# Kernel optimization log

Measured on AMD Instinct MI355X. Metric: run time of the kernel, lower is better.

The kernel has to match this reference:

```python
import jax, jax.numpy as jnp
import numpy as np

B, T, D, H = 8, 1024, 1024, 16

def setup_inputs() -> dict:
    key = jax.random.key(0)
    k1, k2, k3, k4, k5 = jax.random.split(key, 5)
    x = jax.random.normal(k1, (B, T, D), dtype=jnp.float32)
    mask = jnp.tril(jnp.ones((T, T), dtype=bool))[None, None]  # [1,1,T,T] causal
    s = 0.02
    W_attn = jax.random.normal(k2, (D, 3 * D), dtype=jnp.float32) * s
    b_attn = jnp.zeros((3 * D,), dtype=jnp.float32)
    W_proj = jax.random.normal(k3, (D, D), dtype=jnp.float32) * s
    b_proj = jnp.zeros((D,), dtype=jnp.float32)
    return {"x": x, "mask": mask, "W_attn": W_attn, "b_attn": b_attn,
            "W_proj": W_proj, "b_proj": b_proj}

def reference(x, mask, W_attn, b_attn, W_proj, b_proj):
    num_heads = H
    b, t, d = x.shape
    hd = d // num_heads
    qkv = x @ W_attn + b_attn                      # [b,t,3d]
    q, k, v = jnp.split(qkv, 3, axis=-1)
    def to_heads(a):
        return a.reshape(b, t, num_heads, hd).transpose(0, 2, 1, 3)  # [b,h,t,hd]
    q, k, v = to_heads(q), to_heads(k), to_heads(v)
    scale = 1.0 / jnp.sqrt(jnp.float32(hd))
    attn = jnp.einsum('bhqd,bhkd->bhqk', q, k) * scale
    attn = jnp.where(mask, attn, jnp.finfo(jnp.float32).min)
    attn = jax.nn.softmax(attn, axis=-1)
    o = jnp.einsum('bhqk,bhkd->bhqd', attn, v)
    o = o.transpose(0, 2, 1, 3).reshape(b, t, d)   # [b,t,d]
    return o @ W_proj + b_proj
```

## Files before the change

### kernel.cpp

```cpp
#include <hip/hip_runtime.h>
#include <cstdint>


typedef __attribute__((ext_vector_type(8))) short bf16x8;
typedef __attribute__((ext_vector_type(4))) float f32x4;

__device__ __forceinline__ short f2b(float x) {
  unsigned u = __builtin_bit_cast(unsigned, x);
  u += 0x7fffu + ((u >> 16) & 1u);
  return (short)(u >> 16);
}

__device__ __forceinline__ void gl2lds16(short* l, const short* g) {
  __builtin_amdgcn_global_load_lds(
      (const __attribute__((address_space(1))) void*)g,
      (__attribute__((address_space(3))) void*)l, 16, 0, 0);
}


__global__ void f32_to_bf16_vec(const float* __restrict__ in,
                                short* __restrict__ outb, int n4) {
  int i = blockIdx.x * 256 + threadIdx.x;
  if (i >= n4) return;
  float4 v = ((const float4*)in)[i];
  short4 o;
  o.x = f2b(v.x); o.y = f2b(v.y); o.z = f2b(v.z); o.w = f2b(v.w);
  ((short4*)outb)[i] = o;
}

__global__ void transpose_f32_bf16(const float* __restrict__ in,
                                   short* __restrict__ out, int R, int C) {
  __shared__ float tile[32][33];
  int c0 = blockIdx.x * 32, r0 = blockIdx.y * 32;
  int tx = threadIdx.x, ty = threadIdx.y;
#pragma unroll
  for (int i = 0; i < 32; i += 8)
    tile[ty + i][tx] = in[(long)(r0 + ty + i) * C + c0 + tx];
  __syncthreads();
#pragma unroll
  for (int i = 0; i < 32; i += 8)
    out[(long)(c0 + ty + i) * R + r0 + tx] = f2b(tile[tx][ty + i]);
}


template <int EPI>
__global__ __launch_bounds__(256, 3) void gemm_bt(
    const short* __restrict__ A, const short* __restrict__ Bt,
    const float* __restrict__ bias, float* __restrict__ outF,
    short* __restrict__ qh, short* __restrict__ kh, short* __restrict__ vT,
    int M, int N, int K) {
  __shared__ short At[128 * 64];
  __shared__ short Bl[128 * 64];
  const int t = threadIdx.x;
  const int wave = t >> 6, lane = t & 63;
  const int quad = lane >> 4, l15 = lane & 15;
  const int wr = wave >> 1, wc = wave & 1;
  const int m0 = blockIdx.y * 128, n0 = blockIdx.x * 128;

  f32x4 acc[4][4] = {};

  const int srow = t >> 3;
  const int sch0 = t & 7;

  for (int k0 = 0; k0 < K; k0 += 64) {
    __syncthreads();
#pragma unroll
    for (int c = 0; c < 4; ++c) {
      int row = c * 32 + srow;
      int ch = sch0 ^ (row & 7);
      gl2lds16(At + (c * 256 + t) * 8, A + (long)(m0 + row) * K + k0 + ch * 8);
      gl2lds16(Bl + (c * 256 + t) * 8, Bt + (long)(n0 + row) * K + k0 + ch * 8);
    }
    asm volatile("s_waitcnt vmcnt(0)" ::: "memory");
    __syncthreads();

#pragma unroll
    for (int s = 0; s < 2; ++s) {
      const int cx = (s * 4 + quad) ^ (l15 & 7);
      bf16x8 af[4], bfr[4];
#pragma unroll
      for (int i = 0; i < 4; ++i)
        af[i] = *(const bf16x8*)(At + (wr * 64 + i * 16 + l15) * 64 + cx * 8);
#pragma unroll
      for (int j = 0; j < 4; ++j)
        bfr[j] = *(const bf16x8*)(Bl + (wc * 64 + j * 16 + l15) * 64 + cx * 8);
#pragma unroll
      for (int i = 0; i < 4; ++i)
#pragma unroll
        for (int j = 0; j < 4; ++j)
          acc[i][j] = __builtin_amdgcn_mfma_f32_16x16x32_bf16(af[i], bfr[j],
                                                              acc[i][j], 0, 0, 0);
    }
  }

  if (EPI == 1) {
#pragma unroll
    for (int j = 0; j < 4; ++j) {
      int col = n0 + wc * 64 + j * 16 + l15;
      float bv = bias[col];
#pragma unroll
      for (int i = 0; i < 4; ++i)
#pragma unroll
        for (int r = 0; r < 4; ++r) {
          int row = m0 + wr * 64 + i * 16 + quad * 4 + r;
          outF[(long)row * N + col] = acc[i][j][r] + bv;
        }
    }
  } else {
    const int sec = n0 >> 10;
    const int b = m0 >> 10;
#pragma unroll
    for (int j = 0; j < 4; ++j) {
      int col = n0 + wc * 64 + j * 16 + l15;
      float bv = bias[col];
      int d = col & 1023, h = d >> 6, dh = d & 63;
      if (sec == 2) {
        long base = ((long)(b * 16 + h) * 64 + dh) * 1024;
#pragma unroll
        for (int i = 0; i < 4; ++i) {
          int tt0 = (m0 & 1023) + wr * 64 + i * 16 + quad * 4;
          short4 v;
          v.x = f2b(acc[i][j][0] + bv);
          v.y = f2b(acc[i][j][1] + bv);
          v.z = f2b(acc[i][j][2] + bv);
          v.w = f2b(acc[i][j][3] + bv);
          *(short4*)(vT + base + tt0) = v;
        }
      } else {
        short* dst = (sec == 0) ? qh : kh;
        long hbase = ((long)(b * 16 + h) * 1024) * 64 + dh;
#pragma unroll
        for (int i = 0; i < 4; ++i)
#pragma unroll
          for (int r = 0; r < 4; ++r) {
            int tt = (m0 & 1023) + wr * 64 + i * 16 + quad * 4 + r;
            dst[hbase + (long)tt * 64] = f2b(acc[i][j][r] + bv);
          }
      }
    }
  }
}


__global__ __launch_bounds__(256, 2) void attn_kernel(
    const short* __restrict__ qh, const short* __restrict__ kh,
    const short* __restrict__ vT, short* __restrict__ attout) {
  __shared__ short Kb[2][64 * 64];
  __shared__ short Vb[2][64 * 64];
  __shared__ short P_lds[4][16][64];
  const int p = blockIdx.x;
  const int bh = blockIdx.y;
  const int t = threadIdx.x;
  const int wave = t >> 6, lane = t & 63, quad = lane >> 4, l15 = lane & 15;
  const short* q_head = qh + (long)bh * 1024 * 64;
  const short* k_head = kh + (long)bh * 1024 * 64;
  const short* v_head = vT + (long)bh * 64 * 1024;
  const int b_ = bh >> 4, h_ = bh & 15;
  const float sl = 0.125f * 1.44269504089f;

  const int qt[4] = {p, 7 - p, 8 + p, 15 - p};

  auto stage = [&](int kt, int buf) {
    const int kk0 = kt * 64;
#pragma unroll
    for (int i = 0; i < 2; ++i) {
      int s = i * 256 + t;
      int row = s >> 3, cg = (s & 7) ^ (row & 7);
      gl2lds16(&Kb[buf][s * 8], k_head + (kk0 + row) * 64 + cg * 8);
    }
#pragma unroll
    for (int i = 0; i < 2; ++i) {
      int s = i * 256 + t;
      int row = s >> 3, cg = (s & 7) ^ (row & 7);
      gl2lds16(&Vb[buf][s * 8], v_head + row * 1024 + kk0 + cg * 8);
    }
  };

  bf16x8 qf[4][2];
#pragma unroll
  for (int i = 0; i < 4; ++i) {
    int qb = qt[i] * 64 + wave * 16;
#pragma unroll
    for (int s = 0; s < 2; ++s)
      qf[i][s] = *(const bf16x8*)(q_head + (qb + l15) * 64 + s * 32 + quad * 8);
  }

  float l[4][4] = {};
  f32x4 o[4][4] = {};

  stage(0, 0);
  __syncthreads();

  const int nkt = qt[3] + 1;

#pragma unroll 1
  for (int kt = 0; kt < nkt; ++kt) {
    const int buf = kt & 1;
    const short* Kt = Kb[buf];
    const short* Vt = Vb[buf];

    bf16x8 kfr[4][2], vfr[4][2];
#pragma unroll
    for (int jj = 0; jj < 4; ++jj) {
      int row = jj * 16 + l15;
#pragma unroll
      for (int s = 0; s < 2; ++s) {
        int off = ((s * 4 + quad) ^ (row & 7)) * 8;
        kfr[jj][s] = *(const bf16x8*)(Kt + row * 64 + off);
        vfr[jj][s] = *(const bf16x8*)(Vt + row * 64 + off);
      }
    }

    if (kt + 1 < nkt) stage(kt + 1, buf ^ 1);

#pragma unroll
    for (int i = 0; i < 4; ++i) {
      if (kt <= qt[i]) {
        f32x4 s4[4] = {};
#pragma unroll
        for (int jj = 0; jj < 4; ++jj) {
          s4[jj] = __builtin_amdgcn_mfma_f32_16x16x32_bf16(qf[i][0], kfr[jj][0],
                                                           s4[jj], 0, 0, 0);
          s4[jj] = __builtin_amdgcn_mfma_f32_16x16x32_bf16(qf[i][1], kfr[jj][1],
                                                           s4[jj], 0, 0, 0);
        }
        const bool diag = (kt == qt[i]);
        const int qb = qt[i] * 64 + wave * 16;
#pragma unroll
        for (int jj = 0; jj < 4; ++jj) {
          int key = kt * 64 + jj * 16 + l15;
          int ch = jj * 2 + (l15 >> 3), co = l15 & 7;
#pragma unroll
          for (int r = 0; r < 4; ++r) {
            int row = quad * 4 + r;
            float sv = s4[jj][r] * sl;
            if (diag && key > qb + row) sv = -1e30f;
            float e = __builtin_amdgcn_exp2f(sv);
            l[i][r] += e;
            P_lds[wave][row][(ch ^ (row & 7)) * 8 + co] = f2b(e);
          }
        }
        asm volatile("s_waitcnt lgkmcnt(0)" ::: "memory");
        bf16x8 pf[2];
#pragma unroll
        for (int s = 0; s < 2; ++s)
          pf[s] =
              *(const bf16x8*)(&P_lds[wave][l15][((s * 4 + quad) ^ (l15 & 7)) * 8]);
#pragma unroll
        for (int dj = 0; dj < 4; ++dj) {
          o[i][dj] = __builtin_amdgcn_mfma_f32_16x16x32_bf16(pf[0], vfr[dj][0],
                                                             o[i][dj], 0, 0, 0);
          o[i][dj] = __builtin_amdgcn_mfma_f32_16x16x32_bf16(pf[1], vfr[dj][1],
                                                             o[i][dj], 0, 0, 0);
        }
      }
    }
    __syncthreads();
  }

#pragma unroll
  for (int off = 1; off < 16; off <<= 1)
#pragma unroll
    for (int i = 0; i < 4; ++i)
#pragma unroll
      for (int r = 0; r < 4; ++r) l[i][r] += __shfl_xor(l[i][r], off);

  const int erow = lane >> 3, ech = lane & 7;
#pragma unroll
  for (int i = 0; i < 4; ++i) {
    float inv[4];
#pragma unroll
    for (int r = 0; r < 4; ++r) inv[r] = __builtin_amdgcn_rcpf(l[i][r]);
    const int qb = qt[i] * 64 + wave * 16;
#pragma unroll
    for (int dj = 0; dj < 4; ++dj) {
      int ch = dj * 2 + (l15 >> 3), co = l15 & 7;
#pragma unroll
      for (int r = 0; r < 4; ++r) {
        int row = quad * 4 + r;
        P_lds[wave][row][(ch ^ (row & 7)) * 8 + co] = f2b(o[i][dj][r] * inv[r]);
      }
    }
    asm volatile("s_waitcnt lgkmcnt(0)" ::: "memory");
#pragma unroll
    for (int pass = 0; pass < 2; ++pass) {
      int row = pass * 8 + erow;
      bf16x8 v = *(const bf16x8*)(&P_lds[wave][row][(ech ^ (row & 7)) * 8]);
      long g = (long)b_ * 1024 + qb + row;
      *(bf16x8*)(attout + g * 1024 + h_ * 64 + ech * 8) = v;
    }
    asm volatile("s_waitcnt lgkmcnt(0)" ::: "memory");
  }
}


extern "C" void kernel_launch(void* const* d_in, const int* in_sizes, int n_in,
                              void* d_out, int out_size, void* d_ws,
                              size_t ws_size, hipStream_t stream) {
  const float* x = (const float*)d_in[0];
  const float* W_attn = (const float*)d_in[2];
  const float* b_attn = (const float*)d_in[3];
  const float* W_proj = (const float*)d_in[4];
  const float* b_proj = (const float*)d_in[5];
  float* out = (float*)d_out;

  char* ws = (char*)d_ws;
  const size_t MB = 1u << 20;
  short* xb = (short*)(ws);
  short* WaT = (short*)(ws + 16 * MB);
  short* WpT = (short*)(ws + 22 * MB);
  short* qh = (short*)(ws + 24 * MB);
  short* kh = (short*)(ws + 40 * MB);
  short* vT = (short*)(ws + 56 * MB);
  short* attout = xb;

  f32_to_bf16_vec<<<8192, 256, 0, stream>>>(x, xb, 2097152);
  transpose_f32_bf16<<<dim3(3072 / 32, 1024 / 32), dim3(32, 8), 0, stream>>>(
      W_attn, WaT, 1024, 3072);
  transpose_f32_bf16<<<dim3(1024 / 32, 1024 / 32), dim3(32, 8), 0, stream>>>(
      W_proj, WpT, 1024, 1024);
  gemm_bt<0><<<dim3(3072 / 128, 8192 / 128), 256, 0, stream>>>(
      xb, WaT, b_attn, nullptr, qh, kh, vT, 8192, 3072, 1024);
  attn_kernel<<<dim3(4, 128), 256, 0, stream>>>(qh, kh, vT, attout);
  gemm_bt<1><<<dim3(1024 / 128, 8192 / 128), 256, 0, stream>>>(
      attout, WpT, b_proj, out, nullptr, nullptr, nullptr, 8192, 1024, 1024);
}
```

Before: 224.5 us.

## Replace QKV GEMM with 256x256 double-buffered pipelined kernel

Adds a dedicated QKV projection GEMM that uses 256x256 tiles with 512 threads, double-buffered LDS filled by direct global-to-LDS loads, and a four-phase schedule that interleaves the next tile's prefetch with MFMA work. It also remaps block IDs to group neighbouring tiles, aiming for better L2 locality. The intent is higher MFMA utilisation and more operand reuse in the largest GEMM. The cost is higher LDS and register use, and a 12x32 grid of 384 blocks that may leave some compute units underloaded. The output projection GEMM is split out into its own non-templated kernel with the same logic as before.

```diff
diff --git a/kernel.cpp b/kernel.cpp
--- a/kernel.cpp
+++ b/kernel.cpp
@@ -43,11 +43,167 @@
 }
 
 
-template <int EPI>
-__global__ __launch_bounds__(256, 3) void gemm_bt(
+__global__ __launch_bounds__(512, 2) void gemm_qkv256(
+    const short* __restrict__ A, const short* __restrict__ Bt,
+    const float* __restrict__ bias,
+    short* __restrict__ qh, short* __restrict__ kh, short* __restrict__ vT,
+    int M, int N, int K) {
+  __shared__ short As[2][256 * 64];
+  __shared__ short Bs[2][256 * 64];
+  const int t = threadIdx.x;
+  const int wave = t >> 6, lane = t & 63;
+  const int quad = lane >> 4, l15 = lane & 15;
+  const int wm = wave >> 2, wn = wave & 3;
+
+  const int nx = gridDim.x;
+  const int bid0 = blockIdx.y * nx + blockIdx.x;
+  const int cpx = (nx * gridDim.y) >> 3;
+  const int bid = (bid0 & 7) * cpx + (bid0 >> 3);
+  const int n0 = (bid % nx) * 256;
+  const int m0 = (bid / nx) * 256;
+
+  f32x4 acc[8][4] = {};
+
+  const int srow = t >> 3;
+  const int sch = (t & 7) ^ (srow & 7);
+  const short* aS = A + (long)(m0 + srow) * K + sch * 8;
+  const short* bS = Bt + (long)(n0 + srow) * K + sch * 8;
+  const long rK = (long)64 * K;
+
+  const int sw0 = (quad ^ (l15 & 7)) * 8;
+  const int sw1 = ((4 + quad) ^ (l15 & 7)) * 8;
+  const short* aF = &As[0][(wm * 128 + l15) * 64];
+  const short* bF = &Bs[0][(wn * 64 + l15) * 64];
+  const int BUF = 256 * 64;
+
+  const int ntiles = K >> 6;
+
+  {
+    short* ad = &As[0][t * 8];
+    short* bd = &Bs[0][t * 8];
+    gl2lds16(bd, bS);
+    gl2lds16(bd + 4096, bS + rK);
+    gl2lds16(bd + 2 * 4096, bS + 2 * rK);
+    gl2lds16(bd + 3 * 4096, bS + 3 * rK);
+    gl2lds16(ad, aS);
+    gl2lds16(ad + 2 * 4096, aS + 2 * rK);
+    gl2lds16(ad + 4096, aS + rK);
+    gl2lds16(ad + 3 * 4096, aS + 3 * rK);
+  }
+  asm volatile("s_waitcnt vmcnt(2)" ::: "memory");
+  __builtin_amdgcn_s_barrier();
+
+#pragma unroll 1
+  for (int kt = 0; kt < ntiles - 1; ++kt) {
+    const int cur = kt & 1;
+    const short* Ab = aF + cur * BUF;
+    const short* Bb = bF + cur * BUF;
+    short* ad = &As[cur ^ 1][t * 8];
+    short* bd = &Bs[cur ^ 1][t * 8];
+    const short* aN = aS + (long)(kt + 1) * 64;
+    const short* bN = bS + (long)(kt + 1) * 64;
+#pragma unroll
+    for (int ph = 0; ph < 4; ++ph) {
+      const int mh = ph >> 1;
+      const int sw = (ph & 1) ? sw1 : sw0;
+      bf16x8 af[4], bf[4];
+#pragma unroll
+      for (int i = 0; i < 4; ++i)
+        af[i] = *(const bf16x8*)(Ab + (mh * 64 + i * 16) * 64 + sw);
+#pragma unroll
+      for (int j = 0; j < 4; ++j)
+        bf[j] = *(const bf16x8*)(Bb + j * 16 * 64 + sw);
+      if (ph == 0) { gl2lds16(bd, bN); gl2lds16(bd + 4096, bN + rK); }
+      if (ph == 1) { gl2lds16(bd + 2 * 4096, bN + 2 * rK);
+                     gl2lds16(bd + 3 * 4096, bN + 3 * rK); }
+      if (ph == 2) { gl2lds16(ad, aN); gl2lds16(ad + 2 * 4096, aN + 2 * rK); }
+      if (ph == 3) { gl2lds16(ad + 4096, aN + rK);
+                     gl2lds16(ad + 3 * 4096, aN + 3 * rK); }
+      __builtin_amdgcn_s_barrier();
+      asm volatile("s_waitcnt lgkmcnt(0)" ::: "memory");
+      __builtin_amdgcn_sched_barrier(0);
+      __builtin_amdgcn_s_setprio(1);
+#pragma unroll
+      for (int i = 0; i < 4; ++i)
+#pragma unroll
+        for (int j = 0; j < 4; ++j)
+          acc[mh * 4 + i][j] = __builtin_amdgcn_mfma_f32_16x16x32_bf16(
+              af[i], bf[j], acc[mh * 4 + i][j], 0, 0, 0);
+      __builtin_amdgcn_s_setprio(0);
+      if (ph == 1) asm volatile("s_waitcnt vmcnt(4)" ::: "memory");
+      if (ph == 3) asm volatile("s_waitcnt vmcnt(2)" ::: "memory");
+      __builtin_amdgcn_s_barrier();
+    }
+  }
+
+  {
+    const int cur = (ntiles - 1) & 1;
+    const short* Ab = aF + cur * BUF;
+    const short* Bb = bF + cur * BUF;
+#pragma unroll
+    for (int ph = 0; ph < 4; ++ph) {
+      const int mh = ph >> 1;
+      const int sw = (ph & 1) ? sw1 : sw0;
+      bf16x8 af[4], bf[4];
+#pragma unroll
+      for (int i = 0; i < 4; ++i)
+        af[i] = *(const bf16x8*)(Ab + (mh * 64 + i * 16) * 64 + sw);
+#pragma unroll
+      for (int j = 0; j < 4; ++j)
+        bf[j] = *(const bf16x8*)(Bb + j * 16 * 64 + sw);
+      __builtin_amdgcn_s_barrier();
+      asm volatile("s_waitcnt lgkmcnt(0)" ::: "memory");
+      __builtin_amdgcn_sched_barrier(0);
+      __builtin_amdgcn_s_setprio(1);
+#pragma unroll
+      for (int i = 0; i < 4; ++i)
+#pragma unroll
+        for (int j = 0; j < 4; ++j)
+          acc[mh * 4 + i][j] = __builtin_amdgcn_mfma_f32_16x16x32_bf16(
+              af[i], bf[j], acc[mh * 4 + i][j], 0, 0, 0);
+      __builtin_amdgcn_s_setprio(0);
+      if (ph == 1) asm volatile("s_waitcnt vmcnt(0)" ::: "memory");
+      __builtin_amdgcn_s_barrier();
+    }
+  }
+
+  const int sec = n0 >> 10;
+  const int b_ = m0 >> 10;
+#pragma unroll
+  for (int j = 0; j < 4; ++j) {
+    int col = n0 + wn * 64 + j * 16 + l15;
+    float bv = bias[col];
+    int d = col & 1023, h = d >> 6, dh = d & 63;
+    if (sec == 2) {
+      long base = ((long)(b_ * 16 + h) * 64 + dh) * 1024;
+#pragma unroll
+      for (int i = 0; i < 8; ++i) {
+        int tt0 = (m0 & 1023) + wm * 128 + i * 16 + quad * 4;
+        short4 v;
+        v.x = f2b(acc[i][j][0] + bv);
+        v.y = f2b(acc[i][j][1] + bv);
+        v.z = f2b(acc[i][j][2] + bv);
+        v.w = f2b(acc[i][j][3] + bv);
+        *(short4*)(vT + base + tt0) = v;
+      }
+    } else {
+      short* dst = (sec == 0) ? qh : kh;
+      long hbase = ((long)(b_ * 16 + h) * 1024) * 64 + dh;
+#pragma unroll
+      for (int i = 0; i < 8; ++i)
+#pragma unroll
+        for (int r = 0; r < 4; ++r) {
+          int tt = (m0 & 1023) + wm * 128 + i * 16 + quad * 4 + r;
+          dst[hbase + (long)tt * 64] = f2b(acc[i][j][r] + bv);
+        }
+    }
+  }
+}
+
+
+__global__ __launch_bounds__(256, 3) void gemm_proj(
     const short* __restrict__ A, const short* __restrict__ Bt,
     const float* __restrict__ bias, float* __restrict__ outF,
-    short* __restrict__ qh, short* __restrict__ kh, short* __restrict__ vT,
     int M, int N, int K) {
   __shared__ short At[128 * 64];
   __shared__ short Bl[128 * 64];
@@ -93,51 +249,17 @@
     }
   }
 
-  if (EPI == 1) {
-#pragma unroll
-    for (int j = 0; j < 4; ++j) {
-      int col = n0 + wc * 64 + j * 16 + l15;
-      float bv = bias[col];
-#pragma unroll
-      for (int i = 0; i < 4; ++i)
-#pragma unroll
-        for (int r = 0; r < 4; ++r) {
-          int row = m0 + wr * 64 + i * 16 + quad * 4 + r;
-          outF[(long)row * N + col] = acc[i][j][r] + bv;
-        }
-    }
-  } else {
-    const int sec = n0 >> 10;
-    const int b = m0 >> 10;
-#pragma unroll
-    for (int j = 0; j < 4; ++j) {
-      int col = n0 + wc * 64 + j * 16 + l15;
-      float bv = bias[col];
-      int d = col & 1023, h = d >> 6, dh = d & 63;
-      if (sec == 2) {
-        long base = ((long)(b * 16 + h) * 64 + dh) * 1024;
-#pragma unroll
-        for (int i = 0; i < 4; ++i) {
-          int tt0 = (m0 & 1023) + wr * 64 + i * 16 + quad * 4;
-          short4 v;
-          v.x = f2b(acc[i][j][0] + bv);
-          v.y = f2b(acc[i][j][1] + bv);
-          v.z = f2b(acc[i][j][2] + bv);
-          v.w = f2b(acc[i][j][3] + bv);
-          *(short4*)(vT + base + tt0) = v;
-        }
-      } else {
-        short* dst = (sec == 0) ? qh : kh;
-        long hbase = ((long)(b * 16 + h) * 1024) * 64 + dh;
-#pragma unroll
-        for (int i = 0; i < 4; ++i)
-#pragma unroll
-          for (int r = 0; r < 4; ++r) {
-            int tt = (m0 & 1023) + wr * 64 + i * 16 + quad * 4 + r;
-            dst[hbase + (long)tt * 64] = f2b(acc[i][j][r] + bv);
-          }
+#pragma unroll
+  for (int j = 0; j < 4; ++j) {
+    int col = n0 + wc * 64 + j * 16 + l15;
+    float bv = bias[col];
+#pragma unroll
+    for (int i = 0; i < 4; ++i)
+#pragma unroll
+      for (int r = 0; r < 4; ++r) {
+        int row = m0 + wr * 64 + i * 16 + quad * 4 + r;
+        outF[(long)row * N + col] = acc[i][j][r] + bv;
       }
-    }
   }
 }
 
@@ -319,9 +441,9 @@
       W_attn, WaT, 1024, 3072);
   transpose_f32_bf16<<<dim3(1024 / 32, 1024 / 32), dim3(32, 8), 0, stream>>>(
       W_proj, WpT, 1024, 1024);
-  gemm_bt<0><<<dim3(3072 / 128, 8192 / 128), 256, 0, stream>>>(
-      xb, WaT, b_attn, nullptr, qh, kh, vT, 8192, 3072, 1024);
+  gemm_qkv256<<<dim3(3072 / 256, 8192 / 256), 512, 0, stream>>>(
+      xb, WaT, b_attn, qh, kh, vT, 8192, 3072, 1024);
   attn_kernel<<<dim3(4, 128), 256, 0, stream>>>(qh, kh, vT, attout);
-  gemm_bt<1><<<dim3(1024 / 128, 8192 / 128), 256, 0, stream>>>(
-      attout, WpT, b_proj, out, nullptr, nullptr, nullptr, 8192, 1024, 1024);
-}
+  gemm_proj<<<dim3(1024 / 128, 8192 / 128), 256, 0, stream>>>(
+      attout, WpT, b_proj, out, 8192, 1024, 1024);
+}
```

Measured after the change: 240.8 us. 7.3% more time.

## Add 256x256 double-buffered pipelined QKV GEMM with async LDS loads

Applied to the files above, without the earlier changes.

Replaces the 128x128 QKV projection GEMM with a new 512-thread kernel that computes 256x256 output tiles. It double-buffers LDS and issues direct global-to-LDS loads for the next K tiles while MFMA work runs on the current one. Quadrant-wise fragment loads, barriers, explicit waitcnt and s_setprio interleave memory and math, and LDS chunks are XOR-swizzled to avoid bank conflicts. This aims to raise arithmetic intensity and hide load latency, at the cost of 128KB of LDS per block, high register pressure, and a grid of only 384 blocks.

```diff
diff --git a/kernel.cpp b/kernel.cpp
--- a/kernel.cpp
+++ b/kernel.cpp
@@ -40,6 +40,169 @@
 #pragma unroll
   for (int i = 0; i < 32; i += 8)
     out[(long)(c0 + ty + i) * R + r0 + tx] = f2b(tile[tx][ty + i]);
+}
+
+
+__global__ __launch_bounds__(512, 2) void gemm_qkv256(
+    const short* __restrict__ A, const short* __restrict__ Bt,
+    const float* __restrict__ bias,
+    short* __restrict__ qh, short* __restrict__ kh, short* __restrict__ vT,
+    int M, int N, int K) {
+  __shared__ short As[2][256 * 64];
+  __shared__ short Bs[2][256 * 64];
+  const int t = threadIdx.x;
+  const int wave = t >> 6, lane = t & 63;
+  const int quad = lane >> 4, l15 = lane & 15;
+  const int wm = wave >> 2, wn = wave & 3;
+  const int m0 = blockIdx.y * 256, n0 = blockIdx.x * 256;
+
+  f32x4 acc[8][4] = {};
+
+  const int sr = t >> 3;
+  const int sch = (t & 7) ^ (sr & 7);
+  const int brA = sr + (sr & 32);
+  const short* aS = A + (long)(m0 + sr) * K + sch * 8;
+  const short* bSa = Bt + (long)(n0 + brA) * K + sch * 8;
+  const short* bSb = Bt + (long)(n0 + brA + 32) * K + sch * 8;
+  const long K64 = (long)64 * K, K128 = (long)128 * K;
+  const int dBa = brA * 64 + (t & 7) * 8;
+
+  auto stgAa = [&](int tt) {
+    short* d = &As[tt & 1][0];
+    const short* s = aS + (long)tt * 64;
+    gl2lds16(d + t * 8, s);
+    gl2lds16(d + 128 * 64 + t * 8, s + K128);
+  };
+  auto stgAb = [&](int tt) {
+    short* d = &As[tt & 1][0];
+    const short* s = aS + (long)tt * 64 + K64;
+    gl2lds16(d + 64 * 64 + t * 8, s);
+    gl2lds16(d + 192 * 64 + t * 8, s + K128);
+  };
+  auto stgBa = [&](int tt) {
+    short* d = &Bs[tt & 1][0];
+    const short* s = bSa + (long)tt * 64;
+    gl2lds16(d + dBa, s);
+    gl2lds16(d + 128 * 64 + dBa, s + K128);
+  };
+  auto stgBb = [&](int tt) {
+    short* d = &Bs[tt & 1][0];
+    const short* s = bSb + (long)tt * 64;
+    gl2lds16(d + 32 * 64 + dBa, s);
+    gl2lds16(d + 160 * 64 + dBa, s + K128);
+  };
+
+  const int arow = wm * 128 + l15;
+  const int brow = wn * 64 + l15;
+  const int cx0 = (quad ^ (l15 & 7)) * 8;
+  const int cx1 = ((4 + quad) ^ (l15 & 7)) * 8;
+  bf16x8 af[4][2], bfr[2][2];
+
+  auto LDA = [&](const short* Ab, int mh) {
+#pragma unroll
+    for (int i = 0; i < 4; ++i) {
+      const short* p = Ab + (arow + mh * 64 + i * 16) * 64;
+      af[i][0] = *(const bf16x8*)(p + cx0);
+      af[i][1] = *(const bf16x8*)(p + cx1);
+    }
+  };
+  auto LDB = [&](const short* Bb, int nh) {
+#pragma unroll
+    for (int j = 0; j < 2; ++j) {
+      const short* p = Bb + (brow + nh * 32 + j * 16) * 64;
+      bfr[j][0] = *(const bf16x8*)(p + cx0);
+      bfr[j][1] = *(const bf16x8*)(p + cx1);
+    }
+  };
+  auto MF = [&](int mh, int nh) {
+#pragma unroll
+    for (int s = 0; s < 2; ++s)
+#pragma unroll
+      for (int i = 0; i < 4; ++i)
+#pragma unroll
+        for (int j = 0; j < 2; ++j)
+          acc[mh * 4 + i][nh * 2 + j] = __builtin_amdgcn_mfma_f32_16x16x32_bf16(
+              af[i][s], bfr[j][s], acc[mh * 4 + i][nh * 2 + j], 0, 0, 0);
+  };
+
+  auto tileBody = [&](int tt, int mode) {
+    const short* Ab = &As[tt & 1][0];
+    const short* Bb = &Bs[tt & 1][0];
+    LDA(Ab, 0); LDB(Bb, 0);
+    if (mode <= 1) stgBa(tt + 1);
+    __builtin_amdgcn_s_barrier();
+    asm volatile("s_waitcnt lgkmcnt(0)" ::: "memory");
+    __builtin_amdgcn_sched_barrier(0);
+    __builtin_amdgcn_s_setprio(1); MF(0, 0); __builtin_amdgcn_s_setprio(0);
+    __builtin_amdgcn_s_barrier();
+    LDB(Bb, 1);
+    if (mode <= 1) stgAb(tt + 1);
+    __builtin_amdgcn_s_barrier();
+    asm volatile("s_waitcnt lgkmcnt(0)" ::: "memory");
+    __builtin_amdgcn_sched_barrier(0);
+    __builtin_amdgcn_s_setprio(1); MF(0, 1); __builtin_amdgcn_s_setprio(0);
+    if (mode <= 1) asm volatile("s_waitcnt vmcnt(8)" ::: "memory");
+    else asm volatile("s_waitcnt vmcnt(0)" ::: "memory");
+    __builtin_amdgcn_s_barrier();
+    LDA(Ab, 1);
+    if (mode == 0) stgAa(tt + 2);
+    __builtin_amdgcn_s_barrier();
+    asm volatile("s_waitcnt lgkmcnt(0)" ::: "memory");
+    __builtin_amdgcn_sched_barrier(0);
+    __builtin_amdgcn_s_setprio(1); MF(1, 1); __builtin_amdgcn_s_setprio(0);
+    __builtin_amdgcn_s_barrier();
+    LDB(Bb, 0);
+    if (mode == 0) stgBb(tt + 2);
+    __builtin_amdgcn_s_barrier();
+    asm volatile("s_waitcnt lgkmcnt(0)" ::: "memory");
+    __builtin_amdgcn_sched_barrier(0);
+    __builtin_amdgcn_s_setprio(1); MF(1, 0); __builtin_amdgcn_s_setprio(0);
+    if (mode == 0) asm volatile("s_waitcnt vmcnt(6)" ::: "memory");
+    else if (mode == 1) asm volatile("s_waitcnt vmcnt(2)" ::: "memory");
+    __builtin_amdgcn_s_barrier();
+  };
+
+  stgAa(0); stgBb(0); stgBa(0); stgAb(0); stgAa(1); stgBb(1);
+  asm volatile("s_waitcnt vmcnt(6)" ::: "memory");
+  __builtin_amdgcn_s_barrier();
+
+  const int NT = K >> 6;
+#pragma unroll 1
+  for (int tt = 0; tt < NT - 2; ++tt) tileBody(tt, 0);
+  tileBody(NT - 2, 1);
+  tileBody(NT - 1, 2);
+
+  const int sec = n0 >> 10;
+  const int b_ = m0 >> 10;
+#pragma unroll
+  for (int j = 0; j < 4; ++j) {
+    int col = n0 + wn * 64 + j * 16 + l15;
+    float bv = bias[col];
+    int d = col & 1023, h = d >> 6, dh = d & 63;
+    if (sec == 2) {
+      long base = ((long)(b_ * 16 + h) * 64 + dh) * 1024;
+#pragma unroll
+      for (int i = 0; i < 8; ++i) {
+        int tt0 = (m0 & 1023) + wm * 128 + i * 16 + quad * 4;
+        short4 v;
+        v.x = f2b(acc[i][j][0] + bv);
+        v.y = f2b(acc[i][j][1] + bv);
+        v.z = f2b(acc[i][j][2] + bv);
+        v.w = f2b(acc[i][j][3] + bv);
+        *(short4*)(vT + base + tt0) = v;
+      }
+    } else {
+      short* dst = (sec == 0) ? qh : kh;
+      long hbase = ((long)(b_ * 16 + h) * 1024) * 64 + dh;
+#pragma unroll
+      for (int i = 0; i < 8; ++i)
+#pragma unroll
+        for (int r = 0; r < 4; ++r) {
+          int tt = (m0 & 1023) + wm * 128 + i * 16 + quad * 4 + r;
+          dst[hbase + (long)tt * 64] = f2b(acc[i][j][r] + bv);
+        }
+    }
+  }
 }
 
 
@@ -105,38 +268,6 @@
           int row = m0 + wr * 64 + i * 16 + quad * 4 + r;
           outF[(long)row * N + col] = acc[i][j][r] + bv;
         }
-    }
-  } else {
-    const int sec = n0 >> 10;
-    const int b = m0 >> 10;
-#pragma unroll
-    for (int j = 0; j < 4; ++j) {
-      int col = n0 + wc * 64 + j * 16 + l15;
-      float bv = bias[col];
-      int d = col & 1023, h = d >> 6, dh = d & 63;
-      if (sec == 2) {
-        long base = ((long)(b * 16 + h) * 64 + dh) * 1024;
-#pragma unroll
-        for (int i = 0; i < 4; ++i) {
-          int tt0 = (m0 & 1023) + wr * 64 + i * 16 + quad * 4;
-          short4 v;
-          v.x = f2b(acc[i][j][0] + bv);
-          v.y = f2b(acc[i][j][1] + bv);
-          v.z = f2b(acc[i][j][2] + bv);
-          v.w = f2b(acc[i][j][3] + bv);
-          *(short4*)(vT + base + tt0) = v;
-        }
-      } else {
-        short* dst = (sec == 0) ? qh : kh;
-        long hbase = ((long)(b * 16 + h) * 1024) * 64 + dh;
-#pragma unroll
-        for (int i = 0; i < 4; ++i)
-#pragma unroll
-          for (int r = 0; r < 4; ++r) {
-            int tt = (m0 & 1023) + wr * 64 + i * 16 + quad * 4 + r;
-            dst[hbase + (long)tt * 64] = f2b(acc[i][j][r] + bv);
-          }
-      }
     }
   }
 }
@@ -319,8 +450,8 @@
       W_attn, WaT, 1024, 3072);
   transpose_f32_bf16<<<dim3(1024 / 32, 1024 / 32), dim3(32, 8), 0, stream>>>(
       W_proj, WpT, 1024, 1024);
-  gemm_bt<0><<<dim3(3072 / 128, 8192 / 128), 256, 0, stream>>>(
-      xb, WaT, b_attn, nullptr, qh, kh, vT, 8192, 3072, 1024);
+  gemm_qkv256<<<dim3(3072 / 256, 8192 / 256), 512, 0, stream>>>(
+      xb, WaT, b_attn, qh, kh, vT, 8192, 3072, 1024);
   attn_kernel<<<dim3(4, 128), 256, 0, stream>>>(qh, kh, vT, attout);
   gemm_bt<1><<<dim3(1024 / 128, 8192 / 128), 256, 0, stream>>>(
       attout, WpT, b_proj, out, nullptr, nullptr, nullptr, 8192, 1024, 1024);
```

Result: slower. 252.1 us (+12.3%).

## Compute transposed QK^T so P stays in registers, skipping LDS round-trip

Applied to the files above, without the earlier changes.

Swaps the MFMA operand order for the score computation so each lane holds scores for one query and several keys. Those scores can then be packed directly into the A-operand fragments for the PV MFMA, removing the P write to LDS, the wait, and the read back. V fragments are now gathered from LDS with narrower 4-element reads to match the new key layout. Row sums become a single scalar per lane, which reduces the number of shuffles but adds broadcast shuffles at the end, and the narrower V reads raise the LDS instruction count.

```diff
diff --git a/kernel.cpp b/kernel.cpp
--- a/kernel.cpp
+++ b/kernel.cpp
@@ -185,7 +185,7 @@
       qf[i][s] = *(const bf16x8*)(q_head + (qb + l15) * 64 + s * 32 + quad * 8);
   }
 
-  float l[4][4] = {};
+  float l[4] = {};
   f32x4 o[4][4] = {};
 
   stage(0, 0);
@@ -199,7 +199,7 @@
     const short* Kt = Kb[buf];
     const short* Vt = Vb[buf];
 
-    bf16x8 kfr[4][2], vfr[4][2];
+    bf16x8 kfr[4][2];
 #pragma unroll
     for (int jj = 0; jj < 4; ++jj) {
       int row = jj * 16 + l15;
@@ -207,7 +207,26 @@
       for (int s = 0; s < 2; ++s) {
         int off = ((s * 4 + quad) ^ (row & 7)) * 8;
         kfr[jj][s] = *(const bf16x8*)(Kt + row * 64 + off);
-        vfr[jj][s] = *(const bf16x8*)(Vt + row * 64 + off);
+      }
+    }
+    bf16x8 vfr[4][2];
+    {
+      const int qh2 = quad >> 1, ql4 = (quad & 1) * 4;
+#pragma unroll
+      for (int dj = 0; dj < 4; ++dj) {
+        int row = dj * 16 + l15, r7 = row & 7;
+        const short* vr = Vt + row * 64;
+        short4 a0 = *(const short4*)(vr + ((qh2 ^ r7) * 8) + ql4);
+        short4 a1 = *(const short4*)(vr + (((2 + qh2) ^ r7) * 8) + ql4);
+        short4 a2 = *(const short4*)(vr + (((4 + qh2) ^ r7) * 8) + ql4);
+        short4 a3 = *(const short4*)(vr + (((6 + qh2) ^ r7) * 8) + ql4);
+        bf16x8 v0, v1;
+        v0[0] = a0.x; v0[1] = a0.y; v0[2] = a0.z; v0[3] = a0.w;
+        v0[4] = a1.x; v0[5] = a1.y; v0[6] = a1.z; v0[7] = a1.w;
+        v1[0] = a2.x; v1[1] = a2.y; v1[2] = a2.z; v1[3] = a2.w;
+        v1[4] = a3.x; v1[5] = a3.y; v1[6] = a3.z; v1[7] = a3.w;
+        vfr[dj][0] = v0;
+        vfr[dj][1] = v1;
       }
     }
 
@@ -219,38 +238,35 @@
         f32x4 s4[4] = {};
 #pragma unroll
         for (int jj = 0; jj < 4; ++jj) {
-          s4[jj] = __builtin_amdgcn_mfma_f32_16x16x32_bf16(qf[i][0], kfr[jj][0],
+          s4[jj] = __builtin_amdgcn_mfma_f32_16x16x32_bf16(kfr[jj][0], qf[i][0],
                                                            s4[jj], 0, 0, 0);
-          s4[jj] = __builtin_amdgcn_mfma_f32_16x16x32_bf16(qf[i][1], kfr[jj][1],
+          s4[jj] = __builtin_amdgcn_mfma_f32_16x16x32_bf16(kfr[jj][1], qf[i][1],
                                                            s4[jj], 0, 0, 0);
         }
         const bool diag = (kt == qt[i]);
-        const int qb = qt[i] * 64 + wave * 16;
+        const int qg = qt[i] * 64 + wave * 16 + l15;
+        bf16x8 pf0, pf1;
+        float ls = 0.f;
 #pragma unroll
         for (int jj = 0; jj < 4; ++jj) {
-          int key = kt * 64 + jj * 16 + l15;
-          int ch = jj * 2 + (l15 >> 3), co = l15 & 7;
+          const int kbase = kt * 64 + jj * 16 + quad * 4;
 #pragma unroll
           for (int r = 0; r < 4; ++r) {
-            int row = quad * 4 + r;
             float sv = s4[jj][r] * sl;
-            if (diag && key > qb + row) sv = -1e30f;
+            if (diag && (kbase + r) > qg) sv = -1e30f;
             float e = __builtin_amdgcn_exp2f(sv);
-            l[i][r] += e;
-            P_lds[wave][row][(ch ^ (row & 7)) * 8 + co] = f2b(e);
+            ls += e;
+            short bv = f2b(e);
+            if (jj < 2) pf0[(jj & 1) * 4 + r] = bv;
+            else pf1[(jj & 1) * 4 + r] = bv;
           }
         }
-        asm volatile("s_waitcnt lgkmcnt(0)" ::: "memory");
-        bf16x8 pf[2];
-#pragma unroll
-        for (int s = 0; s < 2; ++s)
-          pf[s] =
-              *(const bf16x8*)(&P_lds[wave][l15][((s * 4 + quad) ^ (l15 & 7)) * 8]);
+        l[i] += ls;
 #pragma unroll
         for (int dj = 0; dj < 4; ++dj) {
-          o[i][dj] = __builtin_amdgcn_mfma_f32_16x16x32_bf16(pf[0], vfr[dj][0],
+          o[i][dj] = __builtin_amdgcn_mfma_f32_16x16x32_bf16(pf0, vfr[dj][0],
                                                              o[i][dj], 0, 0, 0);
-          o[i][dj] = __builtin_amdgcn_mfma_f32_16x16x32_bf16(pf[1], vfr[dj][1],
+          o[i][dj] = __builtin_amdgcn_mfma_f32_16x16x32_bf16(pf1, vfr[dj][1],
                                                              o[i][dj], 0, 0, 0);
         }
       }
@@ -259,18 +275,20 @@
   }
 
 #pragma unroll
-  for (int off = 1; off < 16; off <<= 1)
-#pragma unroll
-    for (int i = 0; i < 4; ++i)
-#pragma unroll
-      for (int r = 0; r < 4; ++r) l[i][r] += __shfl_xor(l[i][r], off);
+  for (int i = 0; i < 4; ++i) {
+    l[i] += __shfl_xor(l[i], 16);
+    l[i] += __shfl_xor(l[i], 32);
+  }
 
   const int erow = lane >> 3, ech = lane & 7;
 #pragma unroll
   for (int i = 0; i < 4; ++i) {
     float inv[4];
 #pragma unroll
-    for (int r = 0; r < 4; ++r) inv[r] = __builtin_amdgcn_rcpf(l[i][r]);
+    for (int r = 0; r < 4; ++r) {
+      float lr = __shfl(l[i], quad * 4 + r);
+      inv[r] = __builtin_amdgcn_rcpf(lr);
+    }
     const int qb = qt[i] * 64 + wave * 16;
 #pragma unroll
     for (int dj = 0; dj < 4; ++dj) {
```

Result: slower. 230.1 us (+2.5%).
